# Performance work log

Measured on AMD Instinct MI355X. Metric: run time of the kernel, lower is better.

## Reference

```python
import jax, jax.numpy as jnp
import numpy as np

E, H, V, B, T = 512, 512, 32000, 64, 20


def setup_inputs() -> dict:
    key = jax.random.key(0)
    ks = jax.random.split(key, 10)
    s = 0.05
    return {
        "features": jax.random.normal(ks[0], (B, E), jnp.float32),
        "captions": jax.random.randint(ks[1], (B, T), 0, V),
        "lenghts": jax.random.randint(ks[2], (B,), 1, T),
        "emb_table": jax.random.normal(ks[3], (V, E), jnp.float32) * s,
        "w_ih": jax.random.normal(ks[4], (4 * H, E), jnp.float32) * s,
        "w_hh": jax.random.normal(ks[5], (4 * H, H), jnp.float32) * s,
        "b_ih": jax.random.normal(ks[6], (4 * H,), jnp.float32) * s,
        "b_hh": jax.random.normal(ks[7], (4 * H,), jnp.float32) * s,
        "fc_w": jax.random.normal(ks[8], (V, H), jnp.float32) * s,
        "fc_b": jax.random.normal(ks[9], (V,), jnp.float32) * s,
    }


def _lstm(xs, w_ih, w_hh, b_ih, b_hh):
    # xs: [B, T+1, E] -> hidden states [B, T+1, H], PyTorch gate order i,f,g,o
    b, _, _ = xs.shape
    h0 = jnp.zeros((b, w_hh.shape[1]), xs.dtype)
    c0 = jnp.zeros_like(h0)
    bias = b_ih + b_hh

    def step(carry, x_t):
        h, c = carry
        gates = x_t @ w_ih.T + h @ w_hh.T + bias  # [B, 4H]
        i, f, g, o = jnp.split(gates, 4, axis=-1)
        i, f, o = jax.nn.sigmoid(i), jax.nn.sigmoid(f), jax.nn.sigmoid(o)
        g = jnp.tanh(g)
        c = f * c + i * g
        h = o * jnp.tanh(c)
        return (h, c), h

    _, hs = jax.lax.scan(step, (h0, c0), jnp.swapaxes(xs, 0, 1))  # hs: [T+1, B, H]
    return jnp.swapaxes(hs, 0, 1)


def reference(features, captions, lenghts, emb_table, w_ih, w_hh, b_ih, b_hh, fc_w, fc_b):
    embeddings = emb_table[captions]                       # [B, T, E]
    xs = jnp.concatenate([features[:, None, :], embeddings], axis=1)  # [B, T+1, E]
    hs = _lstm(xs, w_ih, w_hh, b_ih, b_hh)[:, 1:, :]       # [B, T, H]
    logits = hs @ fc_w.T + fc_b                            # [B, T, V]
    # original loops softmax over each 1-D vocab slice == softmax over last axis
    return jax.nn.softmax(logits, axis=-1)
```

## Files before the change

kernel.cpp:

```cpp
#include <hip/hip_runtime.h>
#include <cstdint>
#include <cstddef>

#define E_DIM 512
#define H_DIM 512
#define V_DIM 32000
#define B_DIM 64
#define T_DIM 20
#define NBLK_LSTM 128
#define PT_STRIDE 68

typedef _Float16 f16;
typedef _Float16 f16x8 __attribute__((ext_vector_type(8)));
typedef _Float16 f16x4 __attribute__((ext_vector_type(4)));
typedef float    f32x4 __attribute__((ext_vector_type(4)));

__device__ __forceinline__ void async_lds16(void* lds, const void* g) {
  __builtin_amdgcn_global_load_lds(
      (const __attribute__((address_space(1))) uint32_t*)g,
      (__attribute__((address_space(3))) uint32_t*)lds, 16, 0, 0);
}

__device__ __forceinline__ float sigmoidf_(float x) {
  return 1.0f / (1.0f + expf(-x));
}

__device__ __forceinline__ f16x8 load_h8_coh(const f16* p) {
  union { unsigned long long u[2]; f16x8 v; } r;
  r.u[0] = __hip_atomic_load((const unsigned long long*)p,
                             __ATOMIC_RELAXED, __HIP_MEMORY_SCOPE_AGENT);
  r.u[1] = __hip_atomic_load((const unsigned long long*)(p + 4),
                             __ATOMIC_RELAXED, __HIP_MEMORY_SCOPE_AGENT);
  return r.v;
}
__device__ __forceinline__ void store_h_coh(f16* p, float v) {
  union { f16 h; unsigned short s; } cvt;
  cvt.h = (f16)v;
  __hip_atomic_store((unsigned short*)p, cvt.s,
                     __ATOMIC_RELAXED, __HIP_MEMORY_SCOPE_AGENT);
}

__global__ __launch_bounds__(128) void gather_x16_kernel(
    const float* __restrict__ features, const int* __restrict__ captions,
    const float* __restrict__ emb, f16* __restrict__ x16) {
  const int m = blockIdx.x;
  const int j = threadIdx.x;
  f16x4 r4 = {(f16)0.f, (f16)0.f, (f16)0.f, (f16)0.f};
  if (m < 1344) {
    const int b = m & 63;
    const int t = m >> 6;
    const float* src = (t == 0)
        ? features + (size_t)b * E_DIM
        : emb + (size_t)captions[b * T_DIM + (t - 1)] * E_DIM;
    const float4 v = ((const float4*)src)[j];
    r4.x = (f16)v.x; r4.y = (f16)v.y; r4.z = (f16)v.z; r4.w = (f16)v.w;
  }
  ((f16x4*)(x16 + (size_t)m * 512))[j] = r4;
}

__global__ __launch_bounds__(256) void convert_w_kernel(
    const float* __restrict__ w, f16* __restrict__ w16) {
  const int i = blockIdx.x * 256 + threadIdx.x;
  const float4 v = ((const float4*)w)[i];
  f16x4 r;
  r.x = (f16)v.x; r.y = (f16)v.y; r.z = (f16)v.z; r.w = (f16)v.w;
  ((f16x4*)w16)[i] = r;
}

__global__ __launch_bounds__(256) void bias_sum_kernel(
    const float* __restrict__ a, const float* __restrict__ b,
    float* __restrict__ o) {
  const int i = blockIdx.x * 256 + threadIdx.x;
  if (i < 2048) o[i] = a[i] + b[i];
}

__global__ __launch_bounds__(256) void gemm16_kernel(
    const f16* __restrict__ A, const f16* __restrict__ Bw,
    const float* __restrict__ bias, float* __restrict__ C, int ldc,
    int mode) {
  __shared__ f16 As[128 * 64];
  __shared__ f16 Bs[128 * 64];
  const int tid = threadIdx.x;
  const int lane = tid & 63;
  const int wid = tid >> 6;
  const int m0 = blockIdx.y * 128;
  const int n0 = blockIdx.x * 128;
  const int wm = (wid >> 1) * 64;
  const int wn = (wid & 1) * 64;

  f32x4 acc[4][4];
#pragma unroll
  for (int i = 0; i < 4; ++i)
#pragma unroll
    for (int j = 0; j < 4; ++j) {
      f32x4 z = {0.f, 0.f, 0.f, 0.f};
      acc[i][j] = z;
    }
  const int lr = lane & 15;
  const int lkb = (lane >> 4) * 8;

  for (int kt = 0; kt < 512; kt += 64) {
#pragma unroll
    for (int i = 0; i < 4; ++i) {
      const int off = i * 4096 + wid * 1024 + lane * 16;
      const int row = off >> 7;
      const int colh = (off & 127) >> 1;
      async_lds16((char*)As + i * 4096 + wid * 1024,
                  A + (size_t)(m0 + row) * 512 + kt + colh);
      async_lds16((char*)Bs + i * 4096 + wid * 1024,
                  Bw + (size_t)(n0 + row) * 512 + kt + colh);
    }
    __syncthreads();
#pragma unroll
    for (int ks = 0; ks < 2; ++ks) {
      f16x8 af[4], bf[4];
#pragma unroll
      for (int mi = 0; mi < 4; ++mi)
        af[mi] = *(const f16x8*)&As[(wm + mi * 16 + lr) * 64 + ks * 32 + lkb];
#pragma unroll
      for (int ni = 0; ni < 4; ++ni)
        bf[ni] = *(const f16x8*)&Bs[(wn + ni * 16 + lr) * 64 + ks * 32 + lkb];
#pragma unroll
      for (int mi = 0; mi < 4; ++mi)
#pragma unroll
        for (int ni = 0; ni < 4; ++ni)
          acc[mi][ni] = __builtin_amdgcn_mfma_f32_16x16x32_f16(
              af[mi], bf[ni], acc[mi][ni], 0, 0, 0);
    }
    __syncthreads();
  }

#pragma unroll
  for (int mi = 0; mi < 4; ++mi) {
    const int mbase = m0 + wm + mi * 16 + (lane >> 4) * 4;
#pragma unroll
    for (int ni = 0; ni < 4; ++ni) {
      const int n = n0 + wn + ni * 16 + lr;
      const float bv = bias[n];
#pragma unroll
      for (int r = 0; r < 4; ++r) {
        const int mr = mbase + r;
        size_t off;
        if (mode == 2)
          off = (size_t)(mr >> 6) * (2048 * 64) + (size_t)n * 64 + (mr & 63);
        else if (mode == 1)
          off = (size_t)((mr & 63) * 20 + (mr >> 6)) * ldc + n;
        else
          off = (size_t)mr * ldc + n;
        C[off] = acc[mi][ni][r] + bv;
      }
    }
  }
}

__global__ __launch_bounds__(256) void gemm16_f16out_kernel(
    const f16* __restrict__ A, const f16* __restrict__ Bw,
    const float* __restrict__ bias, f16* __restrict__ C16) {
  __shared__ f16 As[128 * 64];
  __shared__ f16 Bs[128 * 64];
  const int tid = threadIdx.x;
  const int lane = tid & 63;
  const int wid = tid >> 6;
  const int m0 = blockIdx.y * 128;
  const int n0 = blockIdx.x * 128;
  const int wm = (wid >> 1) * 64;
  const int wn = (wid & 1) * 64;

  f32x4 acc[4][4];
#pragma unroll
  for (int i = 0; i < 4; ++i)
#pragma unroll
    for (int j = 0; j < 4; ++j) {
      f32x4 z = {0.f, 0.f, 0.f, 0.f};
      acc[i][j] = z;
    }
  const int lr = lane & 15;
  const int lkb = (lane >> 4) * 8;

  for (int kt = 0; kt < 512; kt += 64) {
#pragma unroll
    for (int i = 0; i < 4; ++i) {
      const int off = i * 4096 + wid * 1024 + lane * 16;
      const int row = off >> 7;
      const int colh = (off & 127) >> 1;
      async_lds16((char*)As + i * 4096 + wid * 1024,
                  A + (size_t)(m0 + row) * 512 + kt + colh);
      async_lds16((char*)Bs + i * 4096 + wid * 1024,
                  Bw + (size_t)(n0 + row) * 512 + kt + colh);
    }
    __syncthreads();
#pragma unroll
    for (int ks = 0; ks < 2; ++ks) {
      f16x8 af[4], bf[4];
#pragma unroll
      for (int mi = 0; mi < 4; ++mi)
        af[mi] = *(const f16x8*)&As[(wm + mi * 16 + lr) * 64 + ks * 32 + lkb];
#pragma unroll
      for (int ni = 0; ni < 4; ++ni)
        bf[ni] = *(const f16x8*)&Bs[(wn + ni * 16 + lr) * 64 + ks * 32 + lkb];
#pragma unroll
      for (int mi = 0; mi < 4; ++mi)
#pragma unroll
        for (int ni = 0; ni < 4; ++ni)
          acc[mi][ni] = __builtin_amdgcn_mfma_f32_16x16x32_f16(
              af[mi], bf[ni], acc[mi][ni], 0, 0, 0);
    }
    __syncthreads();
  }

#pragma unroll
  for (int mi = 0; mi < 4; ++mi) {
    const int mbase = m0 + wm + mi * 16 + (lane >> 4) * 4;
#pragma unroll
    for (int ni = 0; ni < 4; ++ni) {
      const int n = n0 + wn + ni * 16 + lr;
      const float bv = bias[n];
#pragma unroll
      for (int r = 0; r < 4; ++r) {
        const int mr = mbase + r;
        const int orow = (mr & 63) * 20 + (mr >> 6);
        C16[(size_t)orow * 32000 + n] = (f16)(acc[mi][ni][r] + bv);
      }
    }
  }
}

__global__ __launch_bounds__(256, 1) void lstm_persistent5(
    const float* __restrict__ PT, const f16* __restrict__ Whh,
    f16* __restrict__ hsT, unsigned* __restrict__ flags) {
  __shared__ float pS[21 * 16 * PT_STRIDE];
  __shared__ f16 hS[64 * 520];
  const int tid = threadIdx.x;
  const int lane = tid & 63;
  const int w = tid >> 6;
  const int u0 = blockIdx.x * 4;
  const int fr = lane & 15;
  const int fq = lane >> 4;
  const int grow = (fr >> 2) * 512 + u0 + (fr & 3);

  f16x8 bW[16];
  {
    const f16* brow = Whh + (size_t)grow * 512;
#pragma unroll
    for (int kk = 0; kk < 16; ++kk)
      bW[kk] = *(const f16x8*)&brow[kk * 32 + fq * 8];
  }

  for (int i = tid; i < 21 * 16 * 16; i += 256) {
    const int t = i >> 8;
    const int rr = (i & 255) >> 4;
    const int q4 = i & 15;
    const int gr = (rr >> 2) * 512 + u0 + (rr & 3);
    const float4 v = *(const float4*)&PT[((size_t)t * 2048 + gr) * 64 + q4 * 4];
    *(float4*)&pS[(t * 16 + rr) * PT_STRIDE + q4 * 4] = v;
  }
  __syncthreads();

  float cr[4] = {0.f, 0.f, 0.f, 0.f};

  for (int t = 0; t <= T_DIM; ++t) {
    f32x4 acc = {0.f, 0.f, 0.f, 0.f};
    if (t > 0) {
      const f16* src = hsT + (size_t)(t - 1) * (64 * 512)
                           + (size_t)(w * 16) * 512;
      f16x8 hrow[16];
#pragma unroll
      for (int j = 0; j < 16; ++j)
        hrow[j] = load_h8_coh(src + (size_t)j * 512 + lane * 8);
#pragma unroll
      for (int j = 0; j < 16; ++j)
        *(f16x8*)&hS[(w * 16 + j) * 520 + lane * 8] = hrow[j];
      f16x8 a[16];
#pragma unroll
      for (int kk = 0; kk < 16; ++kk)
        a[kk] = *(const f16x8*)&hS[(w * 16 + fr) * 520 + kk * 32 + fq * 8];
#pragma unroll
      for (int kk = 0; kk < 16; ++kk)
        acc = __builtin_amdgcn_mfma_f32_16x16x32_f16(a[kk], bW[kk], acc,
                                                     0, 0, 0);
    }
#pragma unroll
    for (int r = 0; r < 4; ++r) {
      const int b = w * 16 + fq * 4 + r;
      acc[r] += pS[(t * 16 + fr) * PT_STRIDE + b];
    }

    f16* hout = hsT + (size_t)t * (64 * 512);
#pragma unroll
    for (int r = 0; r < 4; ++r) {
      const float x  = acc[r];
      const float xf = __shfl_xor(x, 4);
      const float xg = __shfl_xor(x, 8);
      const float xo = __shfl_xor(x, 12);
      if (fr < 4) {
        const int b = w * 16 + fq * 4 + r;
        const int u = u0 + fr;
        const float si = sigmoidf_(x);
        const float sf = sigmoidf_(xf);
        const float tg = tanhf(xg);
        const float so = sigmoidf_(xo);
        const float cn = sf * cr[r] + si * tg;
        cr[r] = cn;
        const float hn = so * tanhf(cn);
        store_h_coh(&hout[(size_t)b * 512 + u], hn);
      }
    }

    if (t < T_DIM) {
      asm volatile("s_waitcnt vmcnt(0)" ::: "memory");
      __syncthreads();
      if (tid == 0)
        __hip_atomic_store(&flags[blockIdx.x], (unsigned)(t + 1),
                           __ATOMIC_RELAXED, __HIP_MEMORY_SCOPE_AGENT);
      if (tid < NBLK_LSTM) {
        while (__hip_atomic_load(&flags[tid], __ATOMIC_RELAXED,
                                 __HIP_MEMORY_SCOPE_AGENT) < (unsigned)(t + 1))
          __builtin_amdgcn_s_sleep(2);
      }
      __syncthreads();
    }
  }
}

__device__ __forceinline__ float waveMax(float v) {
#pragma unroll
  for (int o = 32; o > 0; o >>= 1) v = fmaxf(v, __shfl_down(v, o));
  return v;
}
__device__ __forceinline__ float waveSum(float v) {
#pragma unroll
  for (int o = 32; o > 0; o >>= 1) v += __shfl_down(v, o);
  return v;
}

__global__ __launch_bounds__(1024) void softmax_f16_kernel(
    const f16* __restrict__ lg, float* __restrict__ out) {
  const f16x8* L = (const f16x8*)(lg + (size_t)blockIdx.x * V_DIM);
  float4* p4 = (float4*)(out + (size_t)blockIdx.x * V_DIM);
  const int t = threadIdx.x;
  __shared__ float sred[16];

  float4 v[8];
  float m = -1e30f;
#pragma unroll
  for (int j = 0; j < 4; ++j) {
    const int i = j * 1024 + t;
    if (i < 4000) {
      const f16x8 h = L[i];
      v[2 * j].x     = (float)h[0]; v[2 * j].y     = (float)h[1];
      v[2 * j].z     = (float)h[2]; v[2 * j].w     = (float)h[3];
      v[2 * j + 1].x = (float)h[4]; v[2 * j + 1].y = (float)h[5];
      v[2 * j + 1].z = (float)h[6]; v[2 * j + 1].w = (float)h[7];
      m = fmaxf(m, fmaxf(fmaxf(v[2 * j].x, v[2 * j].y),
                         fmaxf(v[2 * j].z, v[2 * j].w)));
      m = fmaxf(m, fmaxf(fmaxf(v[2 * j + 1].x, v[2 * j + 1].y),
                         fmaxf(v[2 * j + 1].z, v[2 * j + 1].w)));
    }
  }
  m = waveMax(m);
  if ((t & 63) == 0) sred[t >> 6] = m;
  __syncthreads();
  float mb = sred[0];
#pragma unroll
  for (int k = 1; k < 16; ++k) mb = fmaxf(mb, sred[k]);
  __syncthreads();

  float s = 0.f;
#pragma unroll
  for (int j = 0; j < 8; ++j) {
    const int i = (j >> 1) * 1024 + t;
    if (i < 4000) {
      v[j].x = expf(v[j].x - mb);
      v[j].y = expf(v[j].y - mb);
      v[j].z = expf(v[j].z - mb);
      v[j].w = expf(v[j].w - mb);
      s += v[j].x + v[j].y + v[j].z + v[j].w;
    }
  }
  s = waveSum(s);
  if ((t & 63) == 0) sred[t >> 6] = s;
  __syncthreads();
  float sb = sred[0];
#pragma unroll
  for (int k = 1; k < 16; ++k) sb += sred[k];
  const float inv = 1.0f / sb;

#pragma unroll
  for (int j = 0; j < 4; ++j) {
    const int i = j * 1024 + t;
    if (i < 4000) {
      float4 a = v[2 * j], b = v[2 * j + 1];
      a.x *= inv; a.y *= inv; a.z *= inv; a.w *= inv;
      b.x *= inv; b.y *= inv; b.z *= inv; b.w *= inv;
      p4[2 * i] = a;
      p4[2 * i + 1] = b;
    }
  }
}

__global__ __launch_bounds__(1024) void softmax_reg_kernel(
    float* __restrict__ out) {
  float4* p4 = (float4*)(out + (size_t)blockIdx.x * V_DIM);
  const int t = threadIdx.x;
  __shared__ float sred[16];
  float4 v[8];
  float m = -1e30f;
#pragma unroll
  for (int j = 0; j < 8; ++j) {
    const int i = j * 1024 + t;
    if (i < 8000) {
      v[j] = p4[i];
      m = fmaxf(m, fmaxf(fmaxf(v[j].x, v[j].y), fmaxf(v[j].z, v[j].w)));
    }
  }
  m = waveMax(m);
  if ((t & 63) == 0) sred[t >> 6] = m;
  __syncthreads();
  float mb = sred[0];
#pragma unroll
  for (int k = 1; k < 16; ++k) mb = fmaxf(mb, sred[k]);
  __syncthreads();
  float s = 0.f;
#pragma unroll
  for (int j = 0; j < 8; ++j) {
    const int i = j * 1024 + t;
    if (i < 8000) {
      v[j].x = expf(v[j].x - mb);
      v[j].y = expf(v[j].y - mb);
      v[j].z = expf(v[j].z - mb);
      v[j].w = expf(v[j].w - mb);
      s += v[j].x + v[j].y + v[j].z + v[j].w;
    }
  }
  s = waveSum(s);
  if ((t & 63) == 0) sred[t >> 6] = s;
  __syncthreads();
  float sb = sred[0];
#pragma unroll
  for (int k = 1; k < 16; ++k) sb += sred[k];
  const float inv = 1.0f / sb;
#pragma unroll
  for (int j = 0; j < 8; ++j) {
    const int i = j * 1024 + t;
    if (i < 8000) {
      float4 o;
      o.x = v[j].x * inv; o.y = v[j].y * inv;
      o.z = v[j].z * inv; o.w = v[j].w * inv;
      p4[i] = o;
    }
  }
}

extern "C" void kernel_launch(void* const* d_in, const int* in_sizes, int n_in,
                              void* d_out, int out_size, void* d_ws, size_t ws_size,
                              hipStream_t stream) {
  const float* features = (const float*)d_in[0];
  const int*   captions = (const int*)d_in[1];
  const float* emb      = (const float*)d_in[3];
  const float* w_ih     = (const float*)d_in[4];
  const float* w_hh     = (const float*)d_in[5];
  const float* b_ih     = (const float*)d_in[6];
  const float* b_hh     = (const float*)d_in[7];
  const float* fc_w     = (const float*)d_in[8];
  const float* fc_b     = (const float*)d_in[9];
  float* out = (float*)d_out;

  char* ws = (char*)d_ws;
  unsigned* flags = (unsigned*)ws; ws += 512;
  f16* hsT = (f16*)ws;  ws += (size_t)21 * B_DIM * H_DIM * 2;
  f16* w16 = (f16*)ws;  ws += (size_t)V_DIM * H_DIM * 2;
  f16* logits16 = (f16*)ws;
  const size_t ws_need_f16logits =
      ((char*)logits16 - (char*)d_ws) + (size_t)1280 * V_DIM * 2;
  const bool use_f16_logits = ws_size >= ws_need_f16logits;

  float* PT    = out;
  f16*   x16   = (f16*)(out + 3000000);
  f16*   wih16 = (f16*)(out + 3400000);
  f16*   whh16 = (f16*)(out + 4000000);
  float* bsum  = out + 4600000;

  hipMemsetAsync(flags, 0, 512, stream);

  gather_x16_kernel<<<1408, 128, 0, stream>>>(features, captions, emb, x16);
  convert_w_kernel<<<1024, 256, 0, stream>>>(w_ih, wih16);
  convert_w_kernel<<<1024, 256, 0, stream>>>(w_hh, whh16);
  convert_w_kernel<<<16000, 256, 0, stream>>>(fc_w, w16);
  bias_sum_kernel<<<8, 256, 0, stream>>>(b_ih, b_hh, bsum);

  gemm16_kernel<<<dim3(16, 11), 256, 0, stream>>>(x16, wih16, bsum, PT, 0, 2);

  lstm_persistent5<<<NBLK_LSTM, 256, 0, stream>>>(PT, whh16, hsT, flags);

  const f16* Afc = hsT + (size_t)B_DIM * H_DIM;
  if (use_f16_logits) {
    gemm16_f16out_kernel<<<dim3(250, 10), 256, 0, stream>>>(Afc, w16, fc_b,
                                                            logits16);
    softmax_f16_kernel<<<1280, 1024, 0, stream>>>(logits16, out);
  } else {
    gemm16_kernel<<<dim3(250, 10), 256, 0, stream>>>(Afc, w16, fc_b, out,
                                                     32000, 1);
    softmax_reg_kernel<<<1280, 1024, 0, stream>>>(out);
  }
}
```

Measured before the change: 334.8 us.

## Shrink persistent LSTM grid to 32 blocks with 16 units per block

The persistent LSTM kernel now runs on 32 blocks instead of 128, and each block owns 16 hidden units instead of 4. Each wave computes four M-tiles across the full batch, so every lane does useful gate math instead of only a quarter of lanes. Hidden outputs are staged in LDS and written as coalesced 4-wide atomic stores, and per-step PT slices are loaded into LDS each step instead of preloading all steps. Flags are padded to separate cache lines. Fewer blocks should make the grid barrier cheaper, but each block now does four times the MFMA work per step, which may lengthen the serial critical path.

```diff
diff --git a/kernel.cpp b/kernel.cpp
--- a/kernel.cpp
+++ b/kernel.cpp
@@ -7,8 +7,8 @@
 #define V_DIM 32000
 #define B_DIM 64
 #define T_DIM 20
-#define NBLK_LSTM 128
-#define PT_STRIDE 68
+#define NBLK 32
+#define PT_LDS 68
 
 typedef _Float16 f16;
 typedef _Float16 f16x8 __attribute__((ext_vector_type(8)));
@@ -33,10 +33,10 @@
                              __ATOMIC_RELAXED, __HIP_MEMORY_SCOPE_AGENT);
   return r.v;
 }
-__device__ __forceinline__ void store_h_coh(f16* p, float v) {
-  union { f16 h; unsigned short s; } cvt;
-  cvt.h = (f16)v;
-  __hip_atomic_store((unsigned short*)p, cvt.s,
+__device__ __forceinline__ void store_h4_coh(f16* p, f16x4 v) {
+  union { f16x4 h; unsigned long long u; } cvt;
+  cvt.h = v;
+  __hip_atomic_store((unsigned long long*)p, cvt.u,
                      __ATOMIC_RELAXED, __HIP_MEMORY_SCOPE_AGENT);
 }
 
@@ -225,18 +225,21 @@
   }
 }
 
-__global__ __launch_bounds__(256, 1) void lstm_persistent5(
+__global__ __launch_bounds__(256, 1) void lstm_persistent6(
     const float* __restrict__ PT, const f16* __restrict__ Whh,
     f16* __restrict__ hsT, unsigned* __restrict__ flags) {
-  __shared__ float pS[21 * 16 * PT_STRIDE];
   __shared__ f16 hS[64 * 520];
+  __shared__ float pT[64 * PT_LDS];
+  __shared__ f16 hS2[64 * 16];
   const int tid = threadIdx.x;
   const int lane = tid & 63;
   const int w = tid >> 6;
-  const int u0 = blockIdx.x * 4;
+  const int u0 = blockIdx.x * 16;
   const int fr = lane & 15;
   const int fq = lane >> 4;
-  const int grow = (fr >> 2) * 512 + u0 + (fr & 3);
+  const int q = fr >> 2;
+  const int jw = fr & 3;
+  const int grow = q * 512 + u0 + w * 4 + jw;
 
   f16x8 bW[16];
   {
@@ -246,20 +249,18 @@
       bW[kk] = *(const f16x8*)&brow[kk * 32 + fq * 8];
   }
 
-  for (int i = tid; i < 21 * 16 * 16; i += 256) {
-    const int t = i >> 8;
-    const int rr = (i & 255) >> 4;
+  for (int i = tid; i < 64 * 16; i += 256) {
+    const int rr = i >> 4;
     const int q4 = i & 15;
-    const int gr = (rr >> 2) * 512 + u0 + (rr & 3);
-    const float4 v = *(const float4*)&PT[((size_t)t * 2048 + gr) * 64 + q4 * 4];
-    *(float4*)&pS[(t * 16 + rr) * PT_STRIDE + q4 * 4] = v;
-  }
-  __syncthreads();
+    const int g = rr >> 4, ul = rr & 15;
+    const float4 v =
+        *(const float4*)&PT[((size_t)(g * 512 + u0 + ul)) * 64 + q4 * 4];
+    *(float4*)&pT[rr * PT_LDS + q4 * 4] = v;
+  }
 
   float cr[4] = {0.f, 0.f, 0.f, 0.f};
 
   for (int t = 0; t <= T_DIM; ++t) {
-    f32x4 acc = {0.f, 0.f, 0.f, 0.f};
     if (t > 0) {
       const f16* src = hsT + (size_t)(t - 1) * (64 * 512)
                            + (size_t)(w * 16) * 512;
@@ -270,52 +271,91 @@
 #pragma unroll
       for (int j = 0; j < 16; ++j)
         *(f16x8*)&hS[(w * 16 + j) * 520 + lane * 8] = hrow[j];
-      f16x8 a[16];
-#pragma unroll
-      for (int kk = 0; kk < 16; ++kk)
-        a[kk] = *(const f16x8*)&hS[(w * 16 + fr) * 520 + kk * 32 + fq * 8];
-#pragma unroll
-      for (int kk = 0; kk < 16; ++kk)
-        acc = __builtin_amdgcn_mfma_f32_16x16x32_f16(a[kk], bW[kk], acc,
-                                                     0, 0, 0);
-    }
+    }
+    __syncthreads();
+
+    f32x4 acc[4];
+#pragma unroll
+    for (int mi = 0; mi < 4; ++mi) {
+      f32x4 z = {0.f, 0.f, 0.f, 0.f};
+      acc[mi] = z;
+    }
+    if (t > 0) {
+#pragma unroll
+      for (int mi = 0; mi < 4; ++mi) {
+        f16x8 a[16];
+#pragma unroll
+        for (int kk = 0; kk < 16; ++kk)
+          a[kk] = *(const f16x8*)&hS[(mi * 16 + fr) * 520 + kk * 32 + fq * 8];
+#pragma unroll
+        for (int kk = 0; kk < 16; ++kk)
+          acc[mi] = __builtin_amdgcn_mfma_f32_16x16x32_f16(a[kk], bW[kk],
+                                                           acc[mi], 0, 0, 0);
+      }
+    }
+    const int prow = (q * 16 + w * 4 + jw) * PT_LDS;
+#pragma unroll
+    for (int mi = 0; mi < 4; ++mi)
+#pragma unroll
+      for (int r = 0; r < 4; ++r)
+        acc[mi][r] += pT[prow + mi * 16 + fq * 4 + r];
+
 #pragma unroll
     for (int r = 0; r < 4; ++r) {
-      const int b = w * 16 + fq * 4 + r;
-      acc[r] += pS[(t * 16 + fr) * PT_STRIDE + b];
-    }
-
-    f16* hout = hsT + (size_t)t * (64 * 512);
-#pragma unroll
-    for (int r = 0; r < 4; ++r) {
-      const float x  = acc[r];
-      const float xf = __shfl_xor(x, 4);
-      const float xg = __shfl_xor(x, 8);
-      const float xo = __shfl_xor(x, 12);
-      if (fr < 4) {
-        const int b = w * 16 + fq * 4 + r;
-        const int u = u0 + fr;
-        const float si = sigmoidf_(x);
-        const float sf = sigmoidf_(xf);
-        const float tg = tanhf(xg);
-        const float so = sigmoidf_(xo);
-        const float cn = sf * cr[r] + si * tg;
-        cr[r] = cn;
-        const float hn = so * tanhf(cn);
-        store_h_coh(&hout[(size_t)b * 512 + u], hn);
+      const float y0 = acc[0][r], y1 = acc[1][r], y2 = acc[2][r],
+                  y3 = acc[3][r];
+      const float f0 = __shfl_xor(y0, 4),  f1 = __shfl_xor(y1, 4),
+                  f2 = __shfl_xor(y2, 4),  f3 = __shfl_xor(y3, 4);
+      const float g0 = __shfl_xor(y0, 8),  g1 = __shfl_xor(y1, 8),
+                  g2 = __shfl_xor(y2, 8),  g3 = __shfl_xor(y3, 8);
+      const float o0 = __shfl_xor(y0, 12), o1 = __shfl_xor(y1, 12),
+                  o2 = __shfl_xor(y2, 12), o3 = __shfl_xor(y3, 12);
+      const float x  = q == 0 ? y0 : q == 1 ? y1 : q == 2 ? y2 : y3;
+      const float xf = q == 0 ? f0 : q == 1 ? f1 : q == 2 ? f2 : f3;
+      const float xg = q == 0 ? g0 : q == 1 ? g1 : q == 2 ? g2 : g3;
+      const float xo = q == 0 ? o0 : q == 1 ? o1 : q == 2 ? o2 : o3;
+      const float gi = q == 0 ? x  : q == 1 ? xf : q == 2 ? xg : xo;
+      const float gf = q == 0 ? xf : q == 1 ? x  : q == 2 ? xo : xg;
+      const float gg = q == 0 ? xg : q == 1 ? xo : q == 2 ? x  : xf;
+      const float go = q == 0 ? xo : q == 1 ? xg : q == 2 ? xf : x;
+      const float si = sigmoidf_(gi);
+      const float sf = sigmoidf_(gf);
+      const float tg = tanhf(gg);
+      const float so = sigmoidf_(go);
+      const float cn = sf * cr[r] + si * tg;
+      cr[r] = cn;
+      const float hn = so * tanhf(cn);
+      const int b = q * 16 + fq * 4 + r;
+      hS2[b * 16 + w * 4 + jw] = (f16)hn;
+    }
+    __syncthreads();
+
+    {
+      f16* slab = hsT + (size_t)t * (64 * 512);
+      const int row = tid >> 2;
+      const int c4 = tid & 3;
+      const f16x4 v = *(const f16x4*)&hS2[row * 16 + c4 * 4];
+      store_h4_coh(slab + (size_t)row * 512 + u0 + c4 * 4, v);
+    }
+
+    if (t < T_DIM) {
+      for (int i = tid; i < 64 * 16; i += 256) {
+        const int rr = i >> 4;
+        const int q4 = i & 15;
+        const int g = rr >> 4, ul = rr & 15;
+        const float4 v = *(const float4*)
+            &PT[((size_t)(t + 1) * 2048 + g * 512 + u0 + ul) * 64 + q4 * 4];
+        *(float4*)&pT[rr * PT_LDS + q4 * 4] = v;
       }
-    }
-
-    if (t < T_DIM) {
       asm volatile("s_waitcnt vmcnt(0)" ::: "memory");
       __syncthreads();
       if (tid == 0)
-        __hip_atomic_store(&flags[blockIdx.x], (unsigned)(t + 1),
+        __hip_atomic_store(&flags[blockIdx.x * 16], (unsigned)(t + 1),
                            __ATOMIC_RELAXED, __HIP_MEMORY_SCOPE_AGENT);
-      if (tid < NBLK_LSTM) {
-        while (__hip_atomic_load(&flags[tid], __ATOMIC_RELAXED,
+      if (tid < NBLK) {
+        while (__hip_atomic_load(&flags[tid * 16], __ATOMIC_RELAXED,
                                  __HIP_MEMORY_SCOPE_AGENT) < (unsigned)(t + 1))
-          __builtin_amdgcn_s_sleep(2);
+          __builtin_amdgcn_s_sleep(3);
       }
       __syncthreads();
     }
@@ -466,7 +506,7 @@
   float* out = (float*)d_out;
 
   char* ws = (char*)d_ws;
-  unsigned* flags = (unsigned*)ws; ws += 512;
+  unsigned* flags = (unsigned*)ws; ws += 2048;
   f16* hsT = (f16*)ws;  ws += (size_t)21 * B_DIM * H_DIM * 2;
   f16* w16 = (f16*)ws;  ws += (size_t)V_DIM * H_DIM * 2;
   f16* logits16 = (f16*)ws;
@@ -480,7 +520,7 @@
   f16*   whh16 = (f16*)(out + 4000000);
   float* bsum  = out + 4600000;
 
-  hipMemsetAsync(flags, 0, 512, stream);
+  hipMemsetAsync(flags, 0, 2048, stream);
 
   gather_x16_kernel<<<1408, 128, 0, stream>>>(features, captions, emb, x16);
   convert_w_kernel<<<1024, 256, 0, stream>>>(w_ih, wih16);
@@ -490,7 +530,7 @@
 
   gemm16_kernel<<<dim3(16, 11), 256, 0, stream>>>(x16, wih16, bsum, PT, 0, 2);
 
-  lstm_persistent5<<<NBLK_LSTM, 256, 0, stream>>>(PT, whh16, hsT, flags);
+  lstm_persistent6<<<NBLK, 256, 0, stream>>>(PT, whh16, hsT, flags);
 
   const f16* Afc = hsT + (size_t)B_DIM * H_DIM;
   if (use_f16_logits) {
```

Result: faster. 325.1 us (-2.9%).
